# Optimization experiments

Measured on AMD Instinct MI355X. Metric: run time of the kernel, lower is better.

## Reference

```python
import jax, jax.numpy as jnp
import numpy as np

X_SIZE = 1024
N_HEADS = 16
N_BASIS = 10
MAX_LEN = 4096
CACHE_KEEP_LEN = 4096
B = 8
T_NEW = 128
T_PREV = 4096
HEAD_DIM = X_SIZE // N_HEADS
LN_EPS = 1e-5


def setup_inputs() -> dict:
    key = jax.random.key(0)
    ks = jax.random.split(key, 9)
    def w(k, shape, s):
        return jax.random.normal(k, shape, dtype=jnp.float32) * s
    inv = 1.0 / np.sqrt(X_SIZE)
    return {
        "X": w(ks[0], (B, T_NEW, X_SIZE), 1.0),
        "cache_K": w(ks[1], (B, T_PREV, X_SIZE), 1.0),
        "cache_V": w(ks[2], (B, T_PREV, X_SIZE), 1.0),
        "Wq": w(ks[3], (X_SIZE, X_SIZE), 0.1 * inv),   # Q_SCALE=0.1 (NormedLinear init scale)
        "bq": jnp.zeros((X_SIZE,), jnp.float32),
        "Wk": w(ks[4], (X_SIZE, X_SIZE), 0.2 * inv),   # K_SCALE=0.2, no bias
        "Wv": w(ks[5], (X_SIZE, X_SIZE), 1.0 * inv),   # V_SCALE*sqrt(scale), no bias
        "Wproj": w(ks[6], (X_SIZE, X_SIZE), 1.0 * inv),
        "bproj": jnp.zeros((X_SIZE,), jnp.float32),
        "Wr": w(ks[7], (X_SIZE, N_BASIS * N_HEADS), 0.1 * inv),  # R_SCALE=0.1
        "br": jnp.zeros((N_BASIS * N_HEADS,), jnp.float32),
        "b_nd": w(ks[8], (N_BASIS, MAX_LEN), 0.2),     # B_SCALE=0.2
        "ln_g": jnp.ones((X_SIZE,), jnp.float32),
        "ln_b": jnp.zeros((X_SIZE,), jnp.float32),
    }


def _split_heads(x, h):
    b, t, e = x.shape
    return x.reshape(b, t, h, e // h).transpose(0, 2, 1, 3).reshape(b * h, t, e // h)


def _merge_heads(x, h):
    bh, t, q = x.shape
    b = bh // h
    return x.reshape(b, h, t, q).transpose(0, 2, 1, 3).reshape(b, t, h * q)


def reference(X, cache_K, cache_V, Wq, bq, Wk, Wv, Wproj, bproj, Wr, br, b_nd, ln_g, ln_b):
    Bsz, t, E = X.shape
    # ln_x
    mu = jnp.mean(X, axis=-1, keepdims=True)
    var = jnp.var(X, axis=-1, keepdims=True)
    Xn = (X - mu) / jnp.sqrt(var + LN_EPS) * ln_g + ln_b
    # projections on new tokens
    Q = Xn @ Wq + bq
    K_new = Xn @ Wk
    V_new = Xn @ Wv
    # update_state: append cache (startfull=max(Tprev-cache_keep_len,0))
    Tprev = cache_K.shape[1]
    start = max(Tprev - CACHE_KEEP_LEN, 0)
    Kf = jnp.concatenate([cache_K[:, start:], K_new], axis=1)  # (B, T, E)
    Vf = jnp.concatenate([cache_V[:, start:], V_new], axis=1)
    T = Kf.shape[1]
    Qh = _split_heads(Q, N_HEADS)   # (B*h, t, q)
    Kh = _split_heads(Kf, N_HEADS)  # (B*h, T, q)
    Vh = _split_heads(Vf, N_HEADS)
    # relattn logits: R_btn (B*h, t, n_basis), bandified basis D_ntT
    R = _split_heads(Xn @ Wr + br, N_HEADS)
    d = (T - t + jnp.arange(t)[:, None]) - jnp.arange(T)[None, :]  # (t, T) time diff
    valid = (d >= 0) & (d < MAX_LEN)
    D = jnp.where(valid[None, :, :], b_nd[:, jnp.clip(d, 0, MAX_LEN - 1)], 0.0)  # (n, t, T)
    extra = jnp.einsum('btn,ntT->btT', R, D)  # (B*h, t, T)
    # causal band bias (mask=None -> default causal mask with maxlen window)
    bias = jnp.where(valid, 0.0, -1e9)[None, :, :]
    logits = bias + extra + jnp.einsum('btq,bTq->btT', Qh, Kh) * (1.0 / np.sqrt(HEAD_DIM))
    W_btT = jax.nn.softmax(logits, axis=-1)
    A = _merge_heads(jnp.einsum('btT,bTq->btq', W_btT, Vh), N_HEADS)  # (B, t, E)
    return X + (A @ Wproj + bproj)
```

## Files before the change

### kernel.cpp

```cpp
#include <hip/hip_runtime.h>
#include <hip/hip_bf16.h>

typedef __bf16 bf16;
typedef __bf16 bf16x8 __attribute__((ext_vector_type(8)));
typedef float f32x4 __attribute__((ext_vector_type(4)));
typedef unsigned short u16;
typedef u16 u16x4 __attribute__((ext_vector_type(4)));

#define MFMA16(a, b, c) __builtin_amdgcn_mfma_f32_16x16x32_bf16(a, b, c, 0, 0, 0)
#define LOG2E 1.44269504f

static __device__ __forceinline__ bf16x8 cvt8(float4 a, float4 b) {
  union { bf16 h[8]; bf16x8 v; } u;
  u.h[0] = (bf16)a.x; u.h[1] = (bf16)a.y; u.h[2] = (bf16)a.z; u.h[3] = (bf16)a.w;
  u.h[4] = (bf16)b.x; u.h[5] = (bf16)b.y; u.h[6] = (bf16)b.z; u.h[7] = (bf16)b.w;
  return u.v;
}

__global__ __launch_bounds__(256) void k_ln(const float* __restrict__ X,
                                            const float* __restrict__ g,
                                            const float* __restrict__ bb,
                                            bf16* __restrict__ Xn) {
  int m = blockIdx.x, t = threadIdx.x;
  const float* row = X + (size_t)m * 1024;
  float4 x = ((const float4*)row)[t];
  float s1 = x.x + x.y + x.z + x.w;
  float s2 = x.x * x.x + x.y * x.y + x.z * x.z + x.w * x.w;
#pragma unroll
  for (int off = 1; off < 64; off <<= 1) {
    s1 += __shfl_xor(s1, off);
    s2 += __shfl_xor(s2, off);
  }
  __shared__ float ws1[4], ws2[4];
  int w = t >> 6;
  if ((t & 63) == 0) { ws1[w] = s1; ws2[w] = s2; }
  __syncthreads();
  s1 = ws1[0] + ws1[1] + ws1[2] + ws1[3];
  s2 = ws2[0] + ws2[1] + ws2[2] + ws2[3];
  float mu = s1 * (1.f / 1024.f);
  float var = s2 * (1.f / 1024.f) - mu * mu;
  float rstd = rsqrtf(var + 1e-5f);
  float4 gg = ((const float4*)g)[t];
  float4 bv = ((const float4*)bb)[t];
  union { bf16 h[4]; u16x4 v; } u;
  u.h[0] = (bf16)((x.x - mu) * rstd * gg.x + bv.x);
  u.h[1] = (bf16)((x.y - mu) * rstd * gg.y + bv.y);
  u.h[2] = (bf16)((x.z - mu) * rstd * gg.z + bv.z);
  u.h[3] = (bf16)((x.w - mu) * rstd * gg.w + bv.w);
  ((u16x4*)(Xn + (size_t)m * 1024))[t] = u.v;
}

__global__ __launch_bounds__(256) void k_convert(const float* __restrict__ Wq,
                                                 const float* __restrict__ Wk,
                                                 const float* __restrict__ Wv,
                                                 const float* __restrict__ Wr,
                                                 const float* __restrict__ Wp,
                                                 bf16* __restrict__ Wt_all,
                                                 bf16* __restrict__ Wpt) {
  __shared__ float tile[64][65];
  int t = threadIdx.x;
  int bn = blockIdx.x / 16, bk = blockIdx.x % 16;
  int n0 = bn * 64, k0 = bk * 64;
#pragma unroll
  for (int it = 0; it < 16; ++it) {
    int idx = t + 256 * it;
    int kl = idx >> 6, nl = idx & 63;
    int n = n0 + nl, k = k0 + kl;
    float v;
    if (n < 1024)       v = Wq[(size_t)k * 1024 + n];
    else if (n < 2048)  v = Wk[(size_t)k * 1024 + (n - 1024)];
    else if (n < 3072)  v = Wv[(size_t)k * 1024 + (n - 2048)];
    else if (n < 3232)  v = Wr[(size_t)k * 160 + (n - 3072)];
    else if (n < 3328)  v = 0.f;
    else                v = Wp[(size_t)k * 1024 + (n - 3328)];
    tile[kl][nl] = v;
  }
  __syncthreads();
#pragma unroll
  for (int it = 0; it < 16; ++it) {
    int idx = t + 256 * it;
    int nl = idx >> 6, kl = idx & 63;
    int n = n0 + nl, k = k0 + kl;
    bf16 v = (bf16)tile[kl][nl];
    if (n < 3328) Wt_all[(size_t)n * 1024 + k] = v;
    else          Wpt[(size_t)(n - 3328) * 1024 + k] = v;
  }
}

template <int MODE>
__global__ __launch_bounds__(256) void k_gemm(const bf16* __restrict__ A,
                                              const bf16* __restrict__ Bw,
                                              bf16* __restrict__ Qb, bf16* __restrict__ Kn,
                                              bf16* __restrict__ Vn, float* __restrict__ Rws,
                                              const float* __restrict__ bq,
                                              const float* __restrict__ br,
                                              float* __restrict__ Out,
                                              const float* __restrict__ bproj,
                                              const float* __restrict__ Xres) {
  __shared__ __align__(16) bf16 As[128][72];
  __shared__ __align__(16) bf16 Bs[128][72];
  int t = threadIdx.x, l = t & 63, wid = t >> 6;
  int ln = l & 15, grp = l >> 4;
  int m0 = blockIdx.y * 128, n0 = blockIdx.x * 128;
  int wr = wid >> 1, wc = wid & 1;
  f32x4 acc[4][4] = {};
  int srow = t >> 1, shalf = (t & 1) * 32;

  for (int kt = 0; kt < 16; ++kt) {
    int k0 = kt * 64;
    const bf16* asrc = A + (size_t)(m0 + srow) * 1024 + k0 + shalf;
    const bf16* bsrc = Bw + (size_t)(n0 + srow) * 1024 + k0 + shalf;
    bf16x8 a0 = ((const bf16x8*)asrc)[0], a1 = ((const bf16x8*)asrc)[1];
    bf16x8 a2 = ((const bf16x8*)asrc)[2], a3 = ((const bf16x8*)asrc)[3];
    bf16x8 b0 = ((const bf16x8*)bsrc)[0], b1 = ((const bf16x8*)bsrc)[1];
    bf16x8 b2 = ((const bf16x8*)bsrc)[2], b3 = ((const bf16x8*)bsrc)[3];
    __syncthreads();
    *(bf16x8*)&As[srow][shalf + 0] = a0;  *(bf16x8*)&As[srow][shalf + 8] = a1;
    *(bf16x8*)&As[srow][shalf + 16] = a2; *(bf16x8*)&As[srow][shalf + 24] = a3;
    *(bf16x8*)&Bs[srow][shalf + 0] = b0;  *(bf16x8*)&Bs[srow][shalf + 8] = b1;
    *(bf16x8*)&Bs[srow][shalf + 16] = b2; *(bf16x8*)&Bs[srow][shalf + 24] = b3;
    __syncthreads();
#pragma unroll
    for (int ks = 0; ks < 2; ++ks) {
      int kk = ks * 32 + grp * 8;
      bf16x8 af[4], bf[4];
#pragma unroll
      for (int is = 0; is < 4; ++is) af[is] = *(const bf16x8*)&As[wr * 64 + is * 16 + ln][kk];
#pragma unroll
      for (int js = 0; js < 4; ++js) bf[js] = *(const bf16x8*)&Bs[wc * 64 + js * 16 + ln][kk];
#pragma unroll
      for (int is = 0; is < 4; ++is)
#pragma unroll
        for (int js = 0; js < 4; ++js) acc[is][js] = MFMA16(af[is], bf[js], acc[is][js]);
    }
  }

#pragma unroll
  for (int is = 0; is < 4; ++is)
#pragma unroll
    for (int js = 0; js < 4; ++js)
#pragma unroll
      for (int r = 0; r < 4; ++r) {
        int m = m0 + wr * 64 + is * 16 + grp * 4 + r;
        int n = n0 + wc * 64 + js * 16 + ln;
        float v = acc[is][js][r];
        if (MODE == 0) {
          int b = m >> 7, il = m & 127;
          if (n < 1024) {
            int h = n >> 6, dm = n & 63;
            Qb[((size_t)(b * 16 + h) * 128 + il) * 64 + dm] = (bf16)((v + bq[n]) * (0.125f * LOG2E));
          } else if (n < 2048) {
            Kn[(size_t)m * 1024 + (n - 1024)] = (bf16)v;
          } else if (n < 3072) {
            Vn[(size_t)m * 1024 + (n - 2048)] = (bf16)v;
          } else if (n < 3232) {
            int e = n - 3072, hh = e / 10, nb = e - hh * 10;
            Rws[((size_t)(b * 16 + hh) * 128 + il) * 10 + nb] = v + br[e];
          }
        } else {
          Out[(size_t)m * 1024 + n] = v + bproj[n] + Xres[(size_t)m * 1024 + n];
        }
      }
}

__global__ __launch_bounds__(256, 3) void k_attn(const float* __restrict__ cacheK,
                                                 const float* __restrict__ cacheV,
                                                 const bf16* __restrict__ Kn,
                                                 const bf16* __restrict__ Vn,
                                                 const bf16* __restrict__ Qb,
                                                 const float* __restrict__ Rws,
                                                 const float* __restrict__ bnd,
                                                 bf16* __restrict__ Opart,
                                                 float* __restrict__ mws,
                                                 float* __restrict__ lws) {
  __shared__ __align__(16) bf16 Ks[2][32][72];
  __shared__ __align__(16) bf16 Vt[2][64][36];
  __shared__ __align__(16) bf16 Gw[4][64][36];
  __shared__ __align__(16) bf16 bTf[480][16];

  int t = threadIdx.x, l = t & 63, w = t >> 6;
  int grp = l >> 4, ln = l & 15;
  int s = blockIdx.x % 12, bh = blockIdx.x / 12;
  int b = bh >> 4, h = bh & 15;
  int jbase = s * 352;
  int dlo0 = 4033 - jbase;

  for (int q = t; q < 480; q += 256) {
    int d = dlo0 - 288 + q;
    d = d < 0 ? 0 : (d > 4095 ? 4095 : d);
#pragma unroll
    for (int n = 0; n < 10; ++n) bTf[q][n] = (bf16)bnd[(size_t)n * 4096 + d];
#pragma unroll
    for (int n = 10; n < 16; ++n) bTf[q][n] = (bf16)0.f;
  }

  int iqb = w * 32 + ln;
  bf16x8 qf[2][2];
  bf16x8 rf[2];
#pragma unroll
  for (int hh = 0; hh < 2; ++hh) {
    const bf16* qrow = Qb + ((size_t)bh * 128 + iqb + hh * 16) * 64;
    qf[hh][0] = *(const bf16x8*)(qrow + grp * 8);
    qf[hh][1] = *(const bf16x8*)(qrow + 32 + grp * 8);
    union { bf16 x[8]; bf16x8 v; } u;
    const float* rrow = Rws + ((size_t)bh * 128 + iqb + hh * 16) * 10;
#pragma unroll
    for (int e = 0; e < 8; ++e) {
      int k = grp * 8 + e;
      u.x[e] = (bf16)(k < 10 ? rrow[k] * LOG2E : 0.f);
    }
    rf[hh] = u.v;
  }

  int krow = t >> 3, kcb = (t & 7) * 8;
  int vjl = t & 31, vd0 = (t >> 5) * 8;
  int vsp = (((vjl >> 2) & 3) << 3) | (((vjl >> 4) & 1) << 2) | (vjl & 3);

  float4 kA, kB, vA, vB;

  auto issue = [&](int jt0) {
    if (jt0 < 4096) {
      const float* sk = cacheK + ((size_t)(b * 4096 + jt0 + krow)) * 1024 + h * 64 + kcb;
      kA = *(const float4*)sk;
      kB = *(const float4*)(sk + 4);
      const float* sv = cacheV + ((size_t)(b * 4096 + jt0 + vjl)) * 1024 + h * 64 + vd0;
      vA = *(const float4*)sv;
      vB = *(const float4*)(sv + 4);
    } else {
      bf16x8 kN = *(const bf16x8*)(Kn + ((size_t)(b * 128 + (jt0 + krow - 4096))) * 1024 + h * 64 + kcb);
      bf16x8 vN = *(const bf16x8*)(Vn + ((size_t)(b * 128 + (jt0 + vjl - 4096))) * 1024 + h * 64 + vd0);
      kA = make_float4((float)kN[0], (float)kN[1], (float)kN[2], (float)kN[3]);
      kB = make_float4((float)kN[4], (float)kN[5], (float)kN[6], (float)kN[7]);
      vA = make_float4((float)vN[0], (float)vN[1], (float)vN[2], (float)vN[3]);
      vB = make_float4((float)vN[4], (float)vN[5], (float)vN[6], (float)vN[7]);
    }
  };
  auto stage = [&](int p) {
    *(bf16x8*)&Ks[p][krow][kcb] = cvt8(kA, kB);
    Vt[p][vd0 + 0][vsp] = (bf16)vA.x; Vt[p][vd0 + 1][vsp] = (bf16)vA.y;
    Vt[p][vd0 + 2][vsp] = (bf16)vA.z; Vt[p][vd0 + 3][vsp] = (bf16)vA.w;
    Vt[p][vd0 + 4][vsp] = (bf16)vB.x; Vt[p][vd0 + 5][vsp] = (bf16)vB.y;
    Vt[p][vd0 + 6][vsp] = (bf16)vB.z; Vt[p][vd0 + 7][vsp] = (bf16)vB.w;
  };

  issue(jbase);
  stage(0);
  issue(jbase + 32);

  f32x4 Oacc[2][4] = {};
  float m_r[2] = {-1e30f, -1e30f}, l_r[2] = {0.f, 0.f};

  for (int tt = 0; tt < 11; ++tt) {
    int jt0 = jbase + tt * 32;
    int cur = tt & 1;
    __syncthreads();
    if (tt + 1 < 11) stage(cur ^ 1);
    if (tt + 2 < 11) issue(jbase + (tt + 2) * 32);

    bf16x8 kf[2][2];
#pragma unroll
    for (int js = 0; js < 2; ++js)
#pragma unroll
      for (int ks = 0; ks < 2; ++ks)
        kf[js][ks] = *(const bf16x8*)&Ks[cur][js * 16 + ln][ks * 32 + grp * 8];

    __builtin_amdgcn_s_setprio(1);
    f32x4 Sacc[2][2] = {};
#pragma unroll
    for (int hh = 0; hh < 2; ++hh)
#pragma unroll
      for (int ks = 0; ks < 2; ++ks)
#pragma unroll
        for (int js = 0; js < 2; ++js)
          Sacc[hh][js] = MFMA16(kf[js][ks], qf[hh][ks], Sacc[hh][js]);

    int qb = 320 - 32 * tt + w * 32;
#pragma unroll
    for (int hh = 0; hh < 2; ++hh)
#pragma unroll
      for (int u = 0; u < 3; ++u) {
        bf16x8 bfr = *(const bf16x8*)&bTf[qb + hh * 16 + u * 16 + ln][grp * 8];
        f32x4 z = {};
        f32x4 g = MFMA16(rf[hh], bfr, z);
        union { bf16 x[4]; u16x4 v; } uu;
        uu.x[0] = (bf16)g[0]; uu.x[1] = (bf16)g[1];
        uu.x[2] = (bf16)g[2]; uu.x[3] = (bf16)g[3];
        *(u16x4*)&Gw[w][hh * 16 + u * 16 + ln][hh * 16 + grp * 4] = uu.v;
      }
    __builtin_amdgcn_s_setprio(0);

    float mx[2] = {-1e30f, -1e30f};
    if (jt0 >= 128 && jt0 < 4066) {
#pragma unroll
      for (int hh = 0; hh < 2; ++hh)
#pragma unroll
        for (int js = 0; js < 2; ++js)
#pragma unroll
          for (int r = 0; r < 4; ++r) {
            int jj = js * 16 + grp * 4 + r;
            int cl = hh * 16 + ln - jj + 31;
            float v = Sacc[hh][js][r] + (float)Gw[w][cl][hh * 16 + ln];
            Sacc[hh][js][r] = v;
            mx[hh] = fmaxf(mx[hh], v);
          }
    } else {
#pragma unroll
      for (int hh = 0; hh < 2; ++hh)
#pragma unroll
        for (int js = 0; js < 2; ++js)
#pragma unroll
          for (int r = 0; r < 4; ++r) {
            int jj = js * 16 + grp * 4 + r;
            int iq = iqb + hh * 16;
            int d = 4096 + iq - (jt0 + jj);
            bool valid = ((unsigned)d) < 4096u;
            int cl = hh * 16 + ln - jj + 31;
            float g = (float)Gw[w][cl][hh * 16 + ln];
            float v = valid ? (Sacc[hh][js][r] + g) : -1e9f;
            Sacc[hh][js][r] = v;
            mx[hh] = fmaxf(mx[hh], v);
          }
    }
#pragma unroll
    for (int hh = 0; hh < 2; ++hh) {
      mx[hh] = fmaxf(mx[hh], __shfl_xor(mx[hh], 16));
      mx[hh] = fmaxf(mx[hh], __shfl_xor(mx[hh], 32));
    }

    bool ok = (mx[0] <= m_r[0] + 8.f) && (mx[1] <= m_r[1] + 8.f);
    if (!__all(ok)) {
#pragma unroll
      for (int hh = 0; hh < 2; ++hh) {
        float mnew = fmaxf(m_r[hh], mx[hh]);
        float scn = exp2f(m_r[hh] - mnew);
        m_r[hh] = mnew;
        l_r[hh] *= scn;
#pragma unroll
        for (int r = 0; r < 4; ++r) {
          float scr = __shfl(scn, grp * 4 + r, 16);
#pragma unroll
          for (int ds = 0; ds < 4; ++ds) Oacc[hh][ds][r] *= scr;
        }
      }
    }

    union { bf16 x[8]; bf16x8 v; } p[2];
#pragma unroll
    for (int hh = 0; hh < 2; ++hh) {
      float rsl = 0.f;
#pragma unroll
      for (int js = 0; js < 2; ++js)
#pragma unroll
        for (int r = 0; r < 4; ++r) {
          float pv = exp2f(Sacc[hh][js][r] - m_r[hh]);
          rsl += pv;
          p[hh].x[js * 4 + r] = (bf16)pv;
        }
      l_r[hh] += rsl;
    }
    bf16x8 vf[4];
#pragma unroll
    for (int ds = 0; ds < 4; ++ds) vf[ds] = *(const bf16x8*)&Vt[cur][ds * 16 + ln][grp * 8];

    __builtin_amdgcn_s_setprio(1);
#pragma unroll
    for (int hh = 0; hh < 2; ++hh)
#pragma unroll
      for (int ds = 0; ds < 4; ++ds)
        Oacc[hh][ds] = MFMA16(p[hh].v, vf[ds], Oacc[hh][ds]);
    __builtin_amdgcn_s_setprio(0);
  }

#pragma unroll
  for (int hh = 0; hh < 2; ++hh) {
    l_r[hh] += __shfl_xor(l_r[hh], 16);
    l_r[hh] += __shfl_xor(l_r[hh], 32);
  }

  int part = s * 128 + bh;
#pragma unroll
  for (int hh = 0; hh < 2; ++hh)
#pragma unroll
    for (int ds = 0; ds < 4; ++ds)
#pragma unroll
      for (int r = 0; r < 4; ++r) {
        int il = w * 32 + hh * 16 + grp * 4 + r;
        Opart[((size_t)part * 128 + il) * 64 + ds * 16 + ln] = (bf16)Oacc[hh][ds][r];
      }
  if (grp == 0) {
#pragma unroll
    for (int hh = 0; hh < 2; ++hh) {
      mws[(size_t)part * 128 + iqb + hh * 16] = m_r[hh];
      lws[(size_t)part * 128 + iqb + hh * 16] = l_r[hh];
    }
  }
}

__global__ __launch_bounds__(256) void k_combine(const bf16* __restrict__ Opart,
                                                 const float* __restrict__ mws,
                                                 const float* __restrict__ lws,
                                                 bf16* __restrict__ Aout) {
  __shared__ float msh[12][32], lsh[12][32];
  int bh = blockIdx.x, q = blockIdx.y, t = threadIdx.x;
  int b = bh >> 4, h = bh & 15;
  for (int idx = t; idx < 384; idx += 256) {
    int s = idx >> 5, io = idx & 31;
    msh[s][io] = mws[(size_t)(s * 128 + bh) * 128 + q * 32 + io];
    lsh[s][io] = lws[(size_t)(s * 128 + bh) * 128 + q * 32 + io];
  }
  __syncthreads();
  int dm = t & 63, i4 = t >> 6;
  for (int ii = 0; ii < 8; ++ii) {
    int io = i4 * 8 + ii;
    int i = q * 32 + io;
    float M = -1e30f;
#pragma unroll
    for (int s = 0; s < 12; ++s) M = fmaxf(M, msh[s][io]);
    float L = 0.f, acc = 0.f;
#pragma unroll
    for (int s = 0; s < 12; ++s) {
      float wgt = exp2f(msh[s][io] - M);
      L += wgt * lsh[s][io];
      acc += wgt * (float)Opart[((size_t)(s * 128 + bh) * 128 + i) * 64 + dm];
    }
    Aout[((size_t)(b * 128 + i)) * 1024 + h * 64 + dm] = (bf16)(acc / L);
  }
}

extern "C" void kernel_launch(void* const* d_in, const int* in_sizes, int n_in,
                              void* d_out, int out_size, void* d_ws, size_t ws_size,
                              hipStream_t stream) {
  (void)in_sizes; (void)n_in; (void)out_size; (void)ws_size;
  const float* X      = (const float*)d_in[0];
  const float* cacheK = (const float*)d_in[1];
  const float* cacheV = (const float*)d_in[2];
  const float* Wq     = (const float*)d_in[3];
  const float* bq     = (const float*)d_in[4];
  const float* Wk     = (const float*)d_in[5];
  const float* Wv     = (const float*)d_in[6];
  const float* Wproj  = (const float*)d_in[7];
  const float* bproj  = (const float*)d_in[8];
  const float* Wr     = (const float*)d_in[9];
  const float* br     = (const float*)d_in[10];
  const float* bnd    = (const float*)d_in[11];
  const float* lng    = (const float*)d_in[12];
  const float* lnb    = (const float*)d_in[13];
  float* out = (float*)d_out;

  char* ws = (char*)d_ws;
  bf16* Wt_all = (bf16*)ws;  ws += (size_t)3328 * 1024 * 2;
  bf16* Wpt    = (bf16*)ws;  ws += (size_t)1024 * 1024 * 2;
  bf16* Xn     = (bf16*)ws;  ws += (size_t)1024 * 1024 * 2;
  bf16* Qb     = (bf16*)ws;  ws += (size_t)1024 * 1024 * 2;
  bf16* Kn     = (bf16*)ws;  ws += (size_t)1024 * 1024 * 2;
  bf16* Vn     = (bf16*)ws;  ws += (size_t)1024 * 1024 * 2;
  bf16* Aattn  = (bf16*)ws;  ws += (size_t)1024 * 1024 * 2;
  float* Rws   = (float*)ws; ws += (size_t)128 * 128 * 10 * 4;
  float* mws   = (float*)ws; ws += (size_t)12 * 128 * 128 * 4;
  float* lws   = (float*)ws; ws += (size_t)12 * 128 * 128 * 4;
  bf16* Opart  = (bf16*)ws;  ws += (size_t)12 * 128 * 128 * 64 * 2;

  k_convert<<<dim3(68 * 16), 256, 0, stream>>>(Wq, Wk, Wv, Wr, Wproj, Wt_all, Wpt);
  k_ln<<<dim3(1024), 256, 0, stream>>>(X, lng, lnb, Xn);
  k_gemm<0><<<dim3(26, 8), 256, 0, stream>>>(Xn, Wt_all, Qb, Kn, Vn, Rws, bq, br,
                                             nullptr, nullptr, nullptr);
  k_attn<<<dim3(1536), 256, 0, stream>>>(cacheK, cacheV, Kn, Vn, Qb, Rws, bnd,
                                         Opart, mws, lws);
  k_combine<<<dim3(128, 4), 256, 0, stream>>>(Opart, mws, lws, Aattn);
  k_gemm<1><<<dim3(8, 8), 256, 0, stream>>>(Aattn, Wpt, nullptr, nullptr, nullptr,
                                            nullptr, nullptr, nullptr, out, bproj, X);
}
```

Before: 166.8 us.

## Software-pipeline attention loop: overlap next tile QK with previous softmax/PV

Restructures the attention main loop into a two-stage software pipeline. The QK MFMAs for tile t are issued alongside the bias fold, softmax and PV work for tile t-1, using ping-pong score registers. V gets a triple-buffered LDS stage so tile t-1 stays readable while t+1 is staged. The basis table is also shrunk from 16 to 12 columns, so B fragments are loaded as two 8-byte reads, with a small zero pad buffer. This aims to hide MFMA and LDS latency behind exp/VALU work, at the cost of more registers under a 3-wave occupancy bound and more LDS.

Result: slower. 201.1 us (+20.6%).

```diff
diff --git a/kernel.cpp b/kernel.cpp
--- a/kernel.cpp
+++ b/kernel.cpp
@@ -163,6 +163,114 @@
       }
 }
 
+#define QK_PHASE(TT, SC)                                                        \
+  {                                                                             \
+    const bf16* kb = &Ks[(TT) & 1][0][0];                                       \
+    bf16x8 kf00 = *(const bf16x8*)(kb + (size_t)ln * 72 + grp * 8);             \
+    bf16x8 kf01 = *(const bf16x8*)(kb + (size_t)ln * 72 + 32 + grp * 8);        \
+    bf16x8 kf10 = *(const bf16x8*)(kb + (size_t)(16 + ln) * 72 + grp * 8);      \
+    bf16x8 kf11 = *(const bf16x8*)(kb + (size_t)(16 + ln) * 72 + 32 + grp * 8); \
+    f32x4 z_ = {};                                                              \
+    __builtin_amdgcn_s_setprio(1);                                              \
+    SC[0][0] = MFMA16(kf00, qf[0][0], z_);                                      \
+    SC[0][0] = MFMA16(kf01, qf[0][1], SC[0][0]);                                \
+    SC[0][1] = MFMA16(kf10, qf[0][0], z_);                                      \
+    SC[0][1] = MFMA16(kf11, qf[0][1], SC[0][1]);                                \
+    SC[1][0] = MFMA16(kf00, qf[1][0], z_);                                      \
+    SC[1][0] = MFMA16(kf01, qf[1][1], SC[1][0]);                                \
+    SC[1][1] = MFMA16(kf10, qf[1][0], z_);                                      \
+    SC[1][1] = MFMA16(kf11, qf[1][1], SC[1][1]);                                \
+    __builtin_amdgcn_s_setprio(0);                                              \
+  }
+
+#define G_PHASE(TT)                                                             \
+  {                                                                             \
+    int qb_ = 320 - 32 * (TT) + w * 32;                                         \
+    _Pragma("unroll") for (int hh = 0; hh < 2; ++hh)                            \
+    _Pragma("unroll") for (int u = 0; u < 3; ++u) {                             \
+      int row_ = qb_ + hh * 16 + u * 16 + ln;                                   \
+      const u16* src_ = (const u16*)bTf + row_ * 12 + grp * 8;                  \
+      union { uint2 q2[2]; bf16x8 v; } bu_;                                     \
+      bu_.q2[0] = *(const uint2*)src_;                                          \
+      bu_.q2[1] = *(const uint2*)(src_ + 4);                                    \
+      f32x4 z_ = {};                                                            \
+      f32x4 g_ = MFMA16(rf[hh], bu_.v, z_);                                     \
+      union { bf16 x[4]; u16x4 v4; } uu_;                                       \
+      uu_.x[0] = (bf16)g_[0]; uu_.x[1] = (bf16)g_[1];                           \
+      uu_.x[2] = (bf16)g_[2]; uu_.x[3] = (bf16)g_[3];                           \
+      *(u16x4*)&Gw[w][hh * 16 + u * 16 + ln][hh * 16 + grp * 4] = uu_.v4;       \
+    }                                                                           \
+  }
+
+#define FOLD_PHASE(TP, SP)                                                      \
+  {                                                                             \
+    int jt0p = jbase + (TP) * 32;                                               \
+    mx0 = -1e30f; mx1 = -1e30f;                                                 \
+    if (jt0p >= 128 && jt0p < 4066) {                                           \
+      _Pragma("unroll") for (int js = 0; js < 2; ++js)                          \
+      _Pragma("unroll") for (int r = 0; r < 4; ++r) {                           \
+        int jj = js * 16 + grp * 4 + r;                                         \
+        float v0 = SP[0][js][r] + (float)Gw[w][ln - jj + 31][ln];               \
+        float v1 = SP[1][js][r] + (float)Gw[w][16 + ln - jj + 31][16 + ln];     \
+        SP[0][js][r] = v0; SP[1][js][r] = v1;                                   \
+        mx0 = fmaxf(mx0, v0); mx1 = fmaxf(mx1, v1);                             \
+      }                                                                         \
+    } else {                                                                    \
+      _Pragma("unroll") for (int js = 0; js < 2; ++js)                          \
+      _Pragma("unroll") for (int r = 0; r < 4; ++r) {                           \
+        int jj = js * 16 + grp * 4 + r;                                         \
+        int d0 = 4096 + iqb - (jt0p + jj);                                      \
+        int d1 = d0 + 16;                                                       \
+        float g0 = (float)Gw[w][ln - jj + 31][ln];                              \
+        float g1 = (float)Gw[w][16 + ln - jj + 31][16 + ln];                    \
+        float v0 = (((unsigned)d0) < 4096u) ? (SP[0][js][r] + g0) : -1e9f;      \
+        float v1 = (((unsigned)d1) < 4096u) ? (SP[1][js][r] + g1) : -1e9f;      \
+        SP[0][js][r] = v0; SP[1][js][r] = v1;                                   \
+        mx0 = fmaxf(mx0, v0); mx1 = fmaxf(mx1, v1);                             \
+      }                                                                         \
+    }                                                                           \
+    mx0 = fmaxf(mx0, __shfl_xor(mx0, 16));                                      \
+    mx0 = fmaxf(mx0, __shfl_xor(mx0, 32));                                      \
+    mx1 = fmaxf(mx1, __shfl_xor(mx1, 16));                                      \
+    mx1 = fmaxf(mx1, __shfl_xor(mx1, 32));                                      \
+  }
+
+#define SM_PV_PHASE(TP, SP)                                                     \
+  {                                                                             \
+    bool ok_ = (mx0 <= m_r[0] + 8.f) && (mx1 <= m_r[1] + 8.f);                  \
+    if (!__all(ok_)) {                                                          \
+      float mn0 = fmaxf(m_r[0], mx0), mn1 = fmaxf(m_r[1], mx1);                 \
+      float s0_ = exp2f(m_r[0] - mn0), s1_ = exp2f(m_r[1] - mn1);               \
+      m_r[0] = mn0; m_r[1] = mn1;                                               \
+      l_r[0] *= s0_; l_r[1] *= s1_;                                             \
+      _Pragma("unroll") for (int r = 0; r < 4; ++r) {                           \
+        float c0_ = __shfl(s0_, grp * 4 + r, 16);                               \
+        float c1_ = __shfl(s1_, grp * 4 + r, 16);                               \
+        _Pragma("unroll") for (int ds = 0; ds < 4; ++ds) {                      \
+          Oacc[0][ds][r] *= c0_; Oacc[1][ds][r] *= c1_;                         \
+        }                                                                       \
+      }                                                                         \
+    }                                                                           \
+    union { bf16 x[8]; bf16x8 v; } p0_, p1_;                                    \
+    float rs0_ = 0.f, rs1_ = 0.f;                                               \
+    _Pragma("unroll") for (int js = 0; js < 2; ++js)                            \
+    _Pragma("unroll") for (int r = 0; r < 4; ++r) {                             \
+      float e0_ = exp2f(SP[0][js][r] - m_r[0]);                                 \
+      float e1_ = exp2f(SP[1][js][r] - m_r[1]);                                 \
+      rs0_ += e0_; rs1_ += e1_;                                                 \
+      p0_.x[js * 4 + r] = (bf16)e0_; p1_.x[js * 4 + r] = (bf16)e1_;             \
+    }                                                                           \
+    l_r[0] += rs0_; l_r[1] += rs1_;                                             \
+    int pv_ = (TP) % 3;                                                         \
+    __builtin_amdgcn_s_setprio(1);                                              \
+    _Pragma("unroll") for (int ds = 0; ds < 4; ++ds) {                          \
+      bf16x8 vf_ = *(const bf16x8*)&Vt[pv_][ds * 16 + ln][grp * 8];             \
+      Oacc[0][ds] = MFMA16(p0_.v, vf_, Oacc[0][ds]);                            \
+      Oacc[1][ds] = MFMA16(p1_.v, vf_, Oacc[1][ds]);                            \
+    }                                                                           \
+    __builtin_amdgcn_s_setprio(0);                                              \
+  }
+
 __global__ __launch_bounds__(256, 3) void k_attn(const float* __restrict__ cacheK,
                                                  const float* __restrict__ cacheV,
                                                  const bf16* __restrict__ Kn,
@@ -174,9 +282,10 @@
                                                  float* __restrict__ mws,
                                                  float* __restrict__ lws) {
   __shared__ __align__(16) bf16 Ks[2][32][72];
-  __shared__ __align__(16) bf16 Vt[2][64][36];
+  __shared__ __align__(16) bf16 Vt[3][64][36];
   __shared__ __align__(16) bf16 Gw[4][64][36];
-  __shared__ __align__(16) bf16 bTf[480][16];
+  __shared__ __align__(16) bf16 bTf[480][12];
+  __shared__ __align__(16) bf16 bpad[64];
 
   int t = threadIdx.x, l = t & 63, w = t >> 6;
   int grp = l >> 4, ln = l & 15;
@@ -190,9 +299,9 @@
     d = d < 0 ? 0 : (d > 4095 ? 4095 : d);
 #pragma unroll
     for (int n = 0; n < 10; ++n) bTf[q][n] = (bf16)bnd[(size_t)n * 4096 + d];
-#pragma unroll
-    for (int n = 10; n < 16; ++n) bTf[q][n] = (bf16)0.f;
-  }
+    bTf[q][10] = (bf16)0.f; bTf[q][11] = (bf16)0.f;
+  }
+  if (t < 64) bpad[t] = (bf16)0.f;
 
   int iqb = w * 32 + ln;
   bf16x8 qf[2][2];
@@ -235,141 +344,52 @@
       vB = make_float4((float)vN[4], (float)vN[5], (float)vN[6], (float)vN[7]);
     }
   };
-  auto stage = [&](int p) {
-    *(bf16x8*)&Ks[p][krow][kcb] = cvt8(kA, kB);
-    Vt[p][vd0 + 0][vsp] = (bf16)vA.x; Vt[p][vd0 + 1][vsp] = (bf16)vA.y;
-    Vt[p][vd0 + 2][vsp] = (bf16)vA.z; Vt[p][vd0 + 3][vsp] = (bf16)vA.w;
-    Vt[p][vd0 + 4][vsp] = (bf16)vB.x; Vt[p][vd0 + 5][vsp] = (bf16)vB.y;
-    Vt[p][vd0 + 6][vsp] = (bf16)vB.z; Vt[p][vd0 + 7][vsp] = (bf16)vB.w;
+  auto stage = [&](int tile) {
+    int pk = tile & 1, pv = tile % 3;
+    *(bf16x8*)&Ks[pk][krow][kcb] = cvt8(kA, kB);
+    Vt[pv][vd0 + 0][vsp] = (bf16)vA.x; Vt[pv][vd0 + 1][vsp] = (bf16)vA.y;
+    Vt[pv][vd0 + 2][vsp] = (bf16)vA.z; Vt[pv][vd0 + 3][vsp] = (bf16)vA.w;
+    Vt[pv][vd0 + 4][vsp] = (bf16)vB.x; Vt[pv][vd0 + 5][vsp] = (bf16)vB.y;
+    Vt[pv][vd0 + 6][vsp] = (bf16)vB.z; Vt[pv][vd0 + 7][vsp] = (bf16)vB.w;
   };
+
+  f32x4 Oacc[2][4] = {};
+  float m_r[2] = {-1e30f, -1e30f}, l_r[2] = {0.f, 0.f};
+  f32x4 SA[2][2], SB[2][2];
+  float mx0, mx1;
 
   issue(jbase);
   stage(0);
   issue(jbase + 32);
-
-  f32x4 Oacc[2][4] = {};
-  float m_r[2] = {-1e30f, -1e30f}, l_r[2] = {0.f, 0.f};
-
-  for (int tt = 0; tt < 11; ++tt) {
-    int jt0 = jbase + tt * 32;
-    int cur = tt & 1;
-    __syncthreads();
-    if (tt + 1 < 11) stage(cur ^ 1);
-    if (tt + 2 < 11) issue(jbase + (tt + 2) * 32);
-
-    bf16x8 kf[2][2];
-#pragma unroll
-    for (int js = 0; js < 2; ++js)
-#pragma unroll
-      for (int ks = 0; ks < 2; ++ks)
-        kf[js][ks] = *(const bf16x8*)&Ks[cur][js * 16 + ln][ks * 32 + grp * 8];
-
-    __builtin_amdgcn_s_setprio(1);
-    f32x4 Sacc[2][2] = {};
-#pragma unroll
-    for (int hh = 0; hh < 2; ++hh)
-#pragma unroll
-      for (int ks = 0; ks < 2; ++ks)
-#pragma unroll
-        for (int js = 0; js < 2; ++js)
-          Sacc[hh][js] = MFMA16(kf[js][ks], qf[hh][ks], Sacc[hh][js]);
-
-    int qb = 320 - 32 * tt + w * 32;
-#pragma unroll
-    for (int hh = 0; hh < 2; ++hh)
-#pragma unroll
-      for (int u = 0; u < 3; ++u) {
-        bf16x8 bfr = *(const bf16x8*)&bTf[qb + hh * 16 + u * 16 + ln][grp * 8];
-        f32x4 z = {};
-        f32x4 g = MFMA16(rf[hh], bfr, z);
-        union { bf16 x[4]; u16x4 v; } uu;
-        uu.x[0] = (bf16)g[0]; uu.x[1] = (bf16)g[1];
-        uu.x[2] = (bf16)g[2]; uu.x[3] = (bf16)g[3];
-        *(u16x4*)&Gw[w][hh * 16 + u * 16 + ln][hh * 16 + grp * 4] = uu.v;
-      }
-    __builtin_amdgcn_s_setprio(0);
-
-    float mx[2] = {-1e30f, -1e30f};
-    if (jt0 >= 128 && jt0 < 4066) {
-#pragma unroll
-      for (int hh = 0; hh < 2; ++hh)
-#pragma unroll
-        for (int js = 0; js < 2; ++js)
-#pragma unroll
-          for (int r = 0; r < 4; ++r) {
-            int jj = js * 16 + grp * 4 + r;
-            int cl = hh * 16 + ln - jj + 31;
-            float v = Sacc[hh][js][r] + (float)Gw[w][cl][hh * 16 + ln];
-            Sacc[hh][js][r] = v;
-            mx[hh] = fmaxf(mx[hh], v);
-          }
-    } else {
-#pragma unroll
-      for (int hh = 0; hh < 2; ++hh)
-#pragma unroll
-        for (int js = 0; js < 2; ++js)
-#pragma unroll
-          for (int r = 0; r < 4; ++r) {
-            int jj = js * 16 + grp * 4 + r;
-            int iq = iqb + hh * 16;
-            int d = 4096 + iq - (jt0 + jj);
-            bool valid = ((unsigned)d) < 4096u;
-            int cl = hh * 16 + ln - jj + 31;
-            float g = (float)Gw[w][cl][hh * 16 + ln];
-            float v = valid ? (Sacc[hh][js][r] + g) : -1e9f;
-            Sacc[hh][js][r] = v;
-            mx[hh] = fmaxf(mx[hh], v);
-          }
-    }
-#pragma unroll
-    for (int hh = 0; hh < 2; ++hh) {
-      mx[hh] = fmaxf(mx[hh], __shfl_xor(mx[hh], 16));
-      mx[hh] = fmaxf(mx[hh], __shfl_xor(mx[hh], 32));
-    }
-
-    bool ok = (mx[0] <= m_r[0] + 8.f) && (mx[1] <= m_r[1] + 8.f);
-    if (!__all(ok)) {
-#pragma unroll
-      for (int hh = 0; hh < 2; ++hh) {
-        float mnew = fmaxf(m_r[hh], mx[hh]);
-        float scn = exp2f(m_r[hh] - mnew);
-        m_r[hh] = mnew;
-        l_r[hh] *= scn;
-#pragma unroll
-        for (int r = 0; r < 4; ++r) {
-          float scr = __shfl(scn, grp * 4 + r, 16);
-#pragma unroll
-          for (int ds = 0; ds < 4; ++ds) Oacc[hh][ds][r] *= scr;
-        }
-      }
-    }
-
-    union { bf16 x[8]; bf16x8 v; } p[2];
-#pragma unroll
-    for (int hh = 0; hh < 2; ++hh) {
-      float rsl = 0.f;
-#pragma unroll
-      for (int js = 0; js < 2; ++js)
-#pragma unroll
-        for (int r = 0; r < 4; ++r) {
-          float pv = exp2f(Sacc[hh][js][r] - m_r[hh]);
-          rsl += pv;
-          p[hh].x[js * 4 + r] = (bf16)pv;
-        }
-      l_r[hh] += rsl;
-    }
-    bf16x8 vf[4];
-#pragma unroll
-    for (int ds = 0; ds < 4; ++ds) vf[ds] = *(const bf16x8*)&Vt[cur][ds * 16 + ln][grp * 8];
-
-    __builtin_amdgcn_s_setprio(1);
-#pragma unroll
-    for (int hh = 0; hh < 2; ++hh)
-#pragma unroll
-      for (int ds = 0; ds < 4; ++ds)
-        Oacc[hh][ds] = MFMA16(p[hh].v, vf[ds], Oacc[hh][ds]);
-    __builtin_amdgcn_s_setprio(0);
-  }
+  __syncthreads();
+  QK_PHASE(0, SA)
+  G_PHASE(0)
+  stage(1);
+  issue(jbase + 64);
+
+  for (int tp = 1; tp < 11; tp += 2) {
+    {
+      __syncthreads();
+      QK_PHASE(tp, SB)
+      FOLD_PHASE(tp - 1, SA)
+      G_PHASE(tp)
+      SM_PV_PHASE(tp - 1, SA)
+      if (tp + 1 < 11) stage(tp + 1);
+      if (tp + 2 < 11) issue(jbase + (tp + 2) * 32);
+    }
+    {
+      int tq = tp + 1;
+      __syncthreads();
+      QK_PHASE(tq, SA)
+      FOLD_PHASE(tq - 1, SB)
+      G_PHASE(tq)
+      SM_PV_PHASE(tq - 1, SB)
+      if (tq + 1 < 11) stage(tq + 1);
+      if (tq + 2 < 11) issue(jbase + (tq + 2) * 32);
+    }
+  }
+  FOLD_PHASE(10, SA)
+  SM_PV_PHASE(10, SA)
 
 #pragma unroll
   for (int hh = 0; hh < 2; ++hh) {
```
